# Optimization experiments

Measured on AMD Instinct MI355X. Metric: run time of the kernel, lower is better.

Reference implementation:

```python
import jax, jax.numpy as jnp
import numpy as np

EPS = 1e-12

def _pairwise_dist(a, b):
    # a: [B,N,3], b: [B,M,3] -> Euclidean distances [B,N,M]
    d2 = (jnp.sum(a * a, -1)[:, :, None]
          + jnp.sum(b * b, -1)[:, None, :]
          - 2.0 * jnp.einsum('bnd,bmd->bnm', a, b))
    return jnp.sqrt(jnp.maximum(d2, EPS))


def setup_inputs() -> dict:
    key = jax.random.key(0)
    k1, k2, k3 = jax.random.split(key, 3)
    B, N, M = 16, 4096, 1024
    shape_xyz = jax.random.normal(k1, (B, N, 6), dtype=jnp.float32)
    skel_xyz = jax.random.normal(k2, (B, M, 3), dtype=jnp.float32)
    skel_nori = jax.random.normal(k3, (B, M, 3), dtype=jnp.float32)
    return {"shape_xyz": shape_xyz, "skel_xyz": skel_xyz, "skel_nori": skel_nori}


def reference(shape_xyz, skel_xyz, skel_nori):
    normal = shape_xyz[:, :, 3:6]          # [B,N,3]
    pts = shape_xyz[:, :, :3]              # [B,N,3]
    B = skel_nori.shape[0]

    # Chamfer-style closest distances (sum of min Euclidean distances, both ways)
    d_shape2skel = _pairwise_dist(pts, skel_xyz)   # [B,N,M]
    cd1 = jnp.sum(jnp.min(d_shape2skel, axis=2))
    cd2 = jnp.sum(jnp.min(d_shape2skel, axis=1))   # same matrix transposed
    loss_cd = (cd1 + cd2) * 0.0001

    # KNN (k=2) of each skeletal point among shape points (cKDTree equivalent)
    d_skel2shape = jnp.transpose(d_shape2skel, (0, 2, 1))  # [B,M,N]
    _, idx = jax.lax.top_k(-d_skel2shape, 2)               # [B,M,2]

    # Gather normals of the 2 nearest shape points: [B,M,2,3]
    knn_normals = jnp.take_along_axis(normal[:, None, :, :],
                                      idx[:, :, :, None], axis=2)
    dots = jnp.einsum('bmd,bmkd->bmk', skel_nori, knn_normals)  # [B,M,2]
    # |dot| averaged over k, summed over (b, j), divided by batch size
    loss_normal = jnp.sum(jnp.mean(jnp.abs(dots), axis=-1)) / B

    return loss_cd + 0.001 * loss_normal
```

## Files before the change

kernel.cpp:

```cpp
#include <hip/hip_runtime.h>
#include <cfloat>
#include <stdint.h>

#define B_ 16
#define N_ 4096
#define M_ 1024
#define EPS_ 1e-12f

typedef float v2f __attribute__((ext_vector_type(2)));

__device__ __forceinline__ v2f fma2(v2f a, v2f b, v2f c) {
    return __builtin_elementwise_fma(a, b, c);
}
__device__ __forceinline__ v2f splat(float x) { return (v2f){x, x}; }

__device__ __forceinline__ uint32_t umin3(uint32_t a, uint32_t b, uint32_t c) {
    return min(a, min(b, c));
}
__device__ __forceinline__ uint32_t umed3(uint32_t a, uint32_t b, uint32_t c) {
    return max(min(a, b), min(max(a, b), c));
}

__global__ __launch_bounds__(256, 3) void fused_kernel(const float* __restrict__ shape_xyz,
                                                       const float* __restrict__ skel_xyz,
                                                       const float* __restrict__ skel_nori,
                                                       float* __restrict__ out)
{
    __shared__ float ls[8192];
    __shared__ float ws[4];

    const int tid = threadIdx.x;
    float4* A4 = (float4*)ls;
    float4* Bq = (float4*)(ls + 4096);
    float v = 0.0f;

    if (blockIdx.x < 256) {
        const int b    = blockIdx.x >> 4;
        const int tile = blockIdx.x & 15;

        const float4* g4 = (const float4*)(skel_xyz + (size_t)b * M_ * 3);
        const float4 r0 = g4[3 * tid + 0];
        const float4 r1 = g4[3 * tid + 1];
        const float4 r2 = g4[3 * tid + 2];

        const int sA = tid & 15;
        const int gA = tid >> 4;
        const int n0 = tile * 256 + gA * 16;
        const float* p = shape_xyz + ((size_t)b * N_ + n0) * 6;
        float nx[16], ny[16], nz[16], best[16];
#pragma unroll
        for (int k = 0; k < 16; ++k) {
            nx[k] = -p[k * 6 + 0];
            ny[k] = -p[k * 6 + 1];
            nz[k] = -p[k * 6 + 2];
            best[k] = FLT_MAX;
        }

        {
            const float w0 = fmaf(r0.x, r0.x, fmaf(r0.y, r0.y, r0.z * r0.z));
            const float w1 = fmaf(r0.w, r0.w, fmaf(r1.x, r1.x, r1.y * r1.y));
            const float w2 = fmaf(r1.z, r1.z, fmaf(r1.w, r1.w, r2.x * r2.x));
            const float w3 = fmaf(r2.y, r2.y, fmaf(r2.z, r2.z, r2.w * r2.w));
            A4[2 * tid + 0] = make_float4(2*r0.x, 2*r0.w, 2*r0.y, 2*r1.x);
            Bq[2 * tid + 0] = make_float4(2*r0.z, 2*r1.y, w0, w1);
            A4[2 * tid + 1] = make_float4(2*r1.z, 2*r2.y, 2*r1.w, 2*r2.z);
            Bq[2 * tid + 1] = make_float4(2*r2.x, 2*r2.w, w2, w3);
        }
        __syncthreads();

#pragma unroll 4
        for (int j = 0; j < 32; ++j) {
            const float4 a = A4[j * 16 + sA];
            const float4 bq = Bq[j * 16 + sA];
            const v2f sx = {a.x, a.y};
            const v2f sy = {a.z, a.w};
            const v2f sz = {bq.x, bq.y};
            const v2f sw = {bq.z, bq.w};
#pragma unroll
            for (int k = 0; k < 16; ++k) {
                const v2f t = fma2(splat(nx[k]), sx,
                              fma2(splat(ny[k]), sy,
                              fma2(splat(nz[k]), sz, sw)));
                best[k] = fminf(best[k], fminf(t.x, t.y));
            }
        }

#pragma unroll
        for (int off = 1; off < 16; off <<= 1) {
#pragma unroll
            for (int k = 0; k < 16; ++k) best[k] = fminf(best[k], __shfl_xor(best[k], off));
        }
        if (sA == 0) {
#pragma unroll
            for (int k = 0; k < 16; ++k) {
                const float pp = fmaf(nx[k], nx[k], fmaf(ny[k], ny[k], nz[k] * nz[k]));
                v += sqrtf(fmaxf(best[k] + pp, EPS_));
            }
            v *= 1e-4f;
        }
    } else {
        const int id  = blockIdx.x - 256;
        const int b   = id >> 5;
        const int sub = id & 31;
        const int s   = tid & 31;
        const int g   = tid >> 5;
        const int m0  = sub * 32 + g * 4;

        float m2x[4], m2y[4], m2z[4], aa[4];
        uint32_t k1[4], k2[4];
        {
            const float* sq = skel_xyz + ((size_t)b * M_ + m0) * 3;
#pragma unroll
            for (int c = 0; c < 4; ++c) {
                const float x = sq[c * 3 + 0];
                const float y = sq[c * 3 + 1];
                const float z = sq[c * 3 + 2];
                m2x[c] = -2.0f * x; m2y[c] = -2.0f * y; m2z[c] = -2.0f * z;
                aa[c]  = fmaf(x, x, fmaf(y, y, z * z));
                k1[c] = 0xFFFFFFFFu; k2[c] = 0xFFFFFFFFu;
            }
        }
        float amax = fmaxf(fmaxf(aa[0], aa[1]), fmaxf(aa[2], aa[3]));
#pragma unroll
        for (int off = 1; off < 64; off <<= 1) amax = fmaxf(amax, __shfl_xor(amax, off));
        if ((tid & 63) == 0) ws[tid >> 6] = amax;

        const uint32_t HI = 0xFFFFF000u;
        const float* sb = shape_xyz + (size_t)b * N_ * 6;
        const float4* g4 = (const float4*)sb;

        float4 r[12];
#pragma unroll
        for (int k = 0; k < 12; ++k) r[k] = g4[12 * tid + k];

        float C = 0.0f;
        for (int ph = 0; ph < 2; ++ph) {
            __syncthreads();
            if (ph == 0) C = fmaxf(fmaxf(ws[0], ws[1]), fmaxf(ws[2], ws[3]));
#pragma unroll
            for (int h = 0; h < 2; ++h) {
                const float4 a0 = r[6 * h + 0], a1 = r[6 * h + 1], a2 = r[6 * h + 2];
                const float4 a3 = r[6 * h + 3], a4 = r[6 * h + 4], a5 = r[6 * h + 5];
                const float w0 = fmaf(a0.x, a0.x, fmaf(a0.y, a0.y, a0.z * a0.z)) + C;
                const float w1 = fmaf(a1.z, a1.z, fmaf(a1.w, a1.w, a2.x * a2.x)) + C;
                const float w2 = fmaf(a3.x, a3.x, fmaf(a3.y, a3.y, a3.z * a3.z)) + C;
                const float w3 = fmaf(a4.z, a4.z, fmaf(a4.w, a4.w, a5.x * a5.x)) + C;
                A4[4 * tid + 2 * h + 0] = make_float4(a0.x, a1.z, a0.y, a1.w);
                Bq[4 * tid + 2 * h + 0] = make_float4(a0.z, a2.x, w0, w1);
                A4[4 * tid + 2 * h + 1] = make_float4(a3.x, a4.z, a3.y, a4.w);
                Bq[4 * tid + 2 * h + 1] = make_float4(a3.z, a5.x, w2, w3);
            }
            __syncthreads();
            if (ph == 0) {
#pragma unroll
                for (int k = 0; k < 12; ++k) r[k] = g4[3072 + 12 * tid + k];
            }
            const uint32_t nb = (uint32_t)(ph * 2048);

#pragma unroll 4
            for (int j = 0; j < 32; ++j) {
                const float4 a = A4[j * 32 + s];
                const float4 bq = Bq[j * 32 + s];
                const v2f qx = {a.x, a.y};
                const v2f qy = {a.z, a.w};
                const v2f qz = {bq.x, bq.y};
                const v2f qw = {bq.z, bq.w};
                const uint32_t gn0 = nb + (uint32_t)(j * 64 + 2 * s);
                const uint32_t gn1 = gn0 + 1u;
#pragma unroll
                for (int c = 0; c < 4; ++c) {
                    const v2f t = fma2(splat(m2x[c]), qx,
                                  fma2(splat(m2y[c]), qy,
                                  fma2(splat(m2z[c]), qz, qw)));
                    const uint32_t kk0 = (__float_as_uint(t.x) & HI) | gn0;
                    const uint32_t kk1 = (__float_as_uint(t.y) & HI) | gn1;
                    k2[c] = min(k2[c], umed3(k1[c], kk0, kk1));
                    k1[c] = umin3(k1[c], kk0, kk1);
                }
            }
        }

#pragma unroll
        for (int off = 1; off < 32; off <<= 1) {
#pragma unroll
            for (int c = 0; c < 4; ++c) {
                const uint32_t o1 = (uint32_t)__shfl_xor((int)k1[c], off);
                const uint32_t o2 = (uint32_t)__shfl_xor((int)k2[c], off);
                const uint32_t nk2 = min(min(k2[c], o2), max(k1[c], o1));
                k1[c] = min(k1[c], o1);
                k2[c] = nk2;
            }
        }

        if (s == 0) {
            const float* no = skel_nori + ((size_t)b * M_ + m0) * 3;
            const float kN = 0.001f * 0.5f / (float)B_;
#pragma unroll
            for (int c = 0; c < 4; ++c) {
                const int i1 = (int)(k1[c] & 0xFFFu);
                const int i2 = (int)(k2[c] & 0xFFFu);
                const float* p1 = sb + (size_t)i1 * 6;
                const float* p2 = sb + (size_t)i2 * 6;
                const float ax = -0.5f * m2x[c], ay = -0.5f * m2y[c], az = -0.5f * m2z[c];
                const float dx = ax - p1[0], dy = ay - p1[1], dz = az - p1[2];
                const float d2 = fmaf(dx, dx, fmaf(dy, dy, dz * dz));
                const float q0 = no[c * 3 + 0], q1 = no[c * 3 + 1], q2 = no[c * 3 + 2];
                const float dot1 = q0 * p1[3] + q1 * p1[4] + q2 * p1[5];
                const float dot2 = q0 * p2[3] + q1 * p2[4] + q2 * p2[5];
                v += sqrtf(fmaxf(d2, EPS_)) * 1e-4f + (fabsf(dot1) + fabsf(dot2)) * kN;
            }
        }
    }

#pragma unroll
    for (int off = 32; off > 0; off >>= 1) v += __shfl_down(v, off);
    __syncthreads();
    if ((tid & 63) == 0) ws[tid >> 6] = v;
    __syncthreads();
    if (tid == 0) atomicAdd(out, ws[0] + ws[1] + ws[2] + ws[3]);
}

extern "C" void kernel_launch(void* const* d_in, const int* in_sizes, int n_in,
                              void* d_out, int out_size, void* d_ws, size_t ws_size,
                              hipStream_t stream) {
    const float* shape_xyz = (const float*)d_in[0];
    const float* skel_xyz  = (const float*)d_in[1];
    const float* skel_nori = (const float*)d_in[2];
    float* out = (float*)d_out;

    hipMemsetAsync(out, 0, sizeof(float), stream);
    fused_kernel<<<768, 256, 0, stream>>>(shape_xyz, skel_xyz, skel_nori, out);
}
```

Baseline: 81.64 us.

## Split KNN work across more blocks with full-wavefront lanes and per-thread offset

The KNN branch now uses 64 lanes (a full wavefront) per group of 4 skeleton points and 16 points per block, so the launch grows from 768 to 1280 blocks. The norm offset C becomes a per-thread value added inside the inner loop instead of a block-wide max shared through LDS, which removes the shuffle reduction and one barrier. The launch_bounds occupancy hint is dropped. In exchange, each block still loads and transposes the full shape point cloud into LDS, so more blocks means more redundant global and LDS traffic, and the inner loop gains extra adds.

```diff
diff --git a/kernel.cpp b/kernel.cpp
--- a/kernel.cpp
+++ b/kernel.cpp
@@ -21,14 +21,13 @@
     return max(min(a, b), min(max(a, b), c));
 }
 
-__global__ __launch_bounds__(256, 3) void fused_kernel(const float* __restrict__ shape_xyz,
-                                                       const float* __restrict__ skel_xyz,
-                                                       const float* __restrict__ skel_nori,
-                                                       float* __restrict__ out)
+__global__ __launch_bounds__(256)
+void fused_kernel(const float* __restrict__ shape_xyz,
+                  const float* __restrict__ skel_xyz,
+                  const float* __restrict__ skel_nori,
+                  float* __restrict__ out)
 {
     __shared__ float ls[8192];
-    __shared__ float ws[4];
-
     const int tid = threadIdx.x;
     float4* A4 = (float4*)ls;
     float4* Bq = (float4*)(ls + 4096);
@@ -99,17 +98,19 @@
             v *= 1e-4f;
         }
     } else {
-        const int id  = blockIdx.x - 256;
-        const int b   = id >> 5;
-        const int sub = id & 31;
-        const int s   = tid & 31;
-        const int g   = tid >> 5;
-        const int m0  = sub * 32 + g * 4;
-
-        float m2x[4], m2y[4], m2z[4], aa[4];
+        const int id = blockIdx.x - 256;
+        const int b  = id >> 6;
+        const int mc = id & 63;
+        const int s  = tid & 63;
+        const int g  = tid >> 6;
+        const int m0 = mc * 16 + g * 4;
+
+        float m2x[4], m2y[4], m2z[4];
         uint32_t k1[4], k2[4];
+        float C;
         {
             const float* sq = skel_xyz + ((size_t)b * M_ + m0) * 3;
+            float aa[4];
 #pragma unroll
             for (int c = 0; c < 4; ++c) {
                 const float x = sq[c * 3 + 0];
@@ -119,11 +120,8 @@
                 aa[c]  = fmaf(x, x, fmaf(y, y, z * z));
                 k1[c] = 0xFFFFFFFFu; k2[c] = 0xFFFFFFFFu;
             }
-        }
-        float amax = fmaxf(fmaxf(aa[0], aa[1]), fmaxf(aa[2], aa[3]));
-#pragma unroll
-        for (int off = 1; off < 64; off <<= 1) amax = fmaxf(amax, __shfl_xor(amax, off));
-        if ((tid & 63) == 0) ws[tid >> 6] = amax;
+            C = fmaxf(fmaxf(aa[0], aa[1]), fmaxf(aa[2], aa[3]));
+        }
 
         const uint32_t HI = 0xFFFFF000u;
         const float* sb = shape_xyz + (size_t)b * N_ * 6;
@@ -133,18 +131,16 @@
 #pragma unroll
         for (int k = 0; k < 12; ++k) r[k] = g4[12 * tid + k];
 
-        float C = 0.0f;
         for (int ph = 0; ph < 2; ++ph) {
-            __syncthreads();
-            if (ph == 0) C = fmaxf(fmaxf(ws[0], ws[1]), fmaxf(ws[2], ws[3]));
+            if (ph) __syncthreads();
 #pragma unroll
             for (int h = 0; h < 2; ++h) {
                 const float4 a0 = r[6 * h + 0], a1 = r[6 * h + 1], a2 = r[6 * h + 2];
                 const float4 a3 = r[6 * h + 3], a4 = r[6 * h + 4], a5 = r[6 * h + 5];
-                const float w0 = fmaf(a0.x, a0.x, fmaf(a0.y, a0.y, a0.z * a0.z)) + C;
-                const float w1 = fmaf(a1.z, a1.z, fmaf(a1.w, a1.w, a2.x * a2.x)) + C;
-                const float w2 = fmaf(a3.x, a3.x, fmaf(a3.y, a3.y, a3.z * a3.z)) + C;
-                const float w3 = fmaf(a4.z, a4.z, fmaf(a4.w, a4.w, a5.x * a5.x)) + C;
+                const float w0 = fmaf(a0.x, a0.x, fmaf(a0.y, a0.y, a0.z * a0.z));
+                const float w1 = fmaf(a1.z, a1.z, fmaf(a1.w, a1.w, a2.x * a2.x));
+                const float w2 = fmaf(a3.x, a3.x, fmaf(a3.y, a3.y, a3.z * a3.z));
+                const float w3 = fmaf(a4.z, a4.z, fmaf(a4.w, a4.w, a5.x * a5.x));
                 A4[4 * tid + 2 * h + 0] = make_float4(a0.x, a1.z, a0.y, a1.w);
                 Bq[4 * tid + 2 * h + 0] = make_float4(a0.z, a2.x, w0, w1);
                 A4[4 * tid + 2 * h + 1] = make_float4(a3.x, a4.z, a3.y, a4.w);
@@ -158,20 +154,20 @@
             const uint32_t nb = (uint32_t)(ph * 2048);
 
 #pragma unroll 4
-            for (int j = 0; j < 32; ++j) {
-                const float4 a = A4[j * 32 + s];
-                const float4 bq = Bq[j * 32 + s];
+            for (int j = 0; j < 16; ++j) {
+                const float4 a = A4[j * 64 + s];
+                const float4 bq = Bq[j * 64 + s];
                 const v2f qx = {a.x, a.y};
                 const v2f qy = {a.z, a.w};
                 const v2f qz = {bq.x, bq.y};
-                const v2f qw = {bq.z, bq.w};
-                const uint32_t gn0 = nb + (uint32_t)(j * 64 + 2 * s);
+                const v2f qw0 = {bq.z + C, bq.w + C};
+                const uint32_t gn0 = nb + (uint32_t)(j * 128 + 2 * s);
                 const uint32_t gn1 = gn0 + 1u;
 #pragma unroll
                 for (int c = 0; c < 4; ++c) {
                     const v2f t = fma2(splat(m2x[c]), qx,
                                   fma2(splat(m2y[c]), qy,
-                                  fma2(splat(m2z[c]), qz, qw)));
+                                  fma2(splat(m2z[c]), qz, qw0)));
                     const uint32_t kk0 = (__float_as_uint(t.x) & HI) | gn0;
                     const uint32_t kk1 = (__float_as_uint(t.y) & HI) | gn1;
                     k2[c] = min(k2[c], umed3(k1[c], kk0, kk1));
@@ -181,7 +177,7 @@
         }
 
 #pragma unroll
-        for (int off = 1; off < 32; off <<= 1) {
+        for (int off = 1; off < 64; off <<= 1) {
 #pragma unroll
             for (int c = 0; c < 4; ++c) {
                 const uint32_t o1 = (uint32_t)__shfl_xor((int)k1[c], off);
@@ -215,9 +211,9 @@
 #pragma unroll
     for (int off = 32; off > 0; off >>= 1) v += __shfl_down(v, off);
     __syncthreads();
-    if ((tid & 63) == 0) ws[tid >> 6] = v;
+    if ((tid & 63) == 0) ls[tid >> 6] = v;
     __syncthreads();
-    if (tid == 0) atomicAdd(out, ws[0] + ws[1] + ws[2] + ws[3]);
+    if (tid == 0) atomicAdd(out, ls[0] + ls[1] + ls[2] + ls[3]);
 }
 
 extern "C" void kernel_launch(void* const* d_in, const int* in_sizes, int n_in,
@@ -229,5 +225,5 @@
     float* out = (float*)d_out;
 
     hipMemsetAsync(out, 0, sizeof(float), stream);
-    fused_kernel<<<768, 256, 0, stream>>>(shape_xyz, skel_xyz, skel_nori, out);
-}
+    fused_kernel<<<1280, 256, 0, stream>>>(shape_xyz, skel_xyz, skel_nori, out);
+}
```

After: 90.21 us. 1.11x slower.
